# Optimization experiments

Measured on AMD Instinct MI355X. Metric: run time of the kernel, lower is better.

Reference implementation:

```python
import jax, jax.numpy as jnp
from jax import lax
import numpy as np

B, T, D, H, C = 64, 256, 1024, 1024, 27


def _lstm_layer(x, Wih, Whh, bih, bhh):
    """Batch-first LSTM layer matching torch.nn.LSTM gate math.
    x: (N, S, Din) -> returns hs: (N, S, H). Gate order: i, f, g, o."""
    N = x.shape[0]
    Hh = Whh.shape[1]
    # precompute input contribution for all steps: (N, S, 4H)
    xg = jnp.einsum('nsd,gd->nsg', x, Wih) + bih + bhh

    def step(carry, xg_t):
        h, c = carry
        g = xg_t + h @ Whh.T  # (N, 4H)
        i, f, gg, o = jnp.split(g, 4, axis=-1)
        c = jax.nn.sigmoid(f) * c + jax.nn.sigmoid(i) * jnp.tanh(gg)
        h = jax.nn.sigmoid(o) * jnp.tanh(c)
        return (h, c), h

    h0 = jnp.zeros((N, Hh), x.dtype)
    (_, _), hs = lax.scan(step, (h0, h0), jnp.swapaxes(xg, 0, 1))  # scan over S
    return jnp.swapaxes(hs, 0, 1)  # (N, S, H)


def setup_inputs() -> dict:
    key = jax.random.key(0)
    ks = jax.random.split(key, 13)
    s = 1.0 / np.sqrt(H)
    u = lambda k, shape: jax.random.uniform(k, shape, jnp.float32, -s, s)
    return {
        'x': jax.random.normal(ks[0], (B, T, D), jnp.float32),
        'Wih0': u(ks[1], (4 * H, D)), 'Whh0': u(ks[2], (4 * H, H)),
        'bih0': u(ks[3], (4 * H,)), 'bhh0': u(ks[4], (4 * H,)),
        'Wih1': u(ks[5], (4 * H, H)), 'Whh1': u(ks[6], (4 * H, H)),
        'bih1': u(ks[7], (4 * H,)), 'bhh1': u(ks[8], (4 * H,)),
        'W1': u(ks[9], (H // 2, H)), 'b1': u(ks[10], (H // 2,)),
        'W2': u(ks[11], (C, H // 2)), 'b2': u(ks[12], (C,)),
    }


def reference(x, Wih0, Whh0, bih0, bhh0, Wih1, Whh1, bih1, bhh1, W1, b1, W2, b2):
    # Original module permutes (B,T,D) -> (T,B,D) but the LSTM is batch_first,
    # so it treats T as batch and recurs over the original batch axis B.
    xp = jnp.transpose(x, (1, 0, 2))           # (T, B, D): batch=T, seq=B
    h1 = _lstm_layer(xp, Wih0, Whh0, bih0, bhh0)  # (T, B, H)
    h2 = _lstm_layer(h1, Wih1, Whh1, bih1, bhh1)  # (T, B, H)
    out = h2[-1]                                # (B, H): last 'batch' row
    fc = jax.nn.relu(out @ W1.T + b1)
    return fc @ W2.T + b2                       # (B, C)
```

## Files before the change

kernel.cpp:

```cpp
#include <hip/hip_runtime.h>
#include <math.h>


#define NBLK 256
#define TPB  512
#define HDIM 1024
#define SEQ  64
#define GUARD (1L << 20)
#define POISON 0xAAAAAAAAu
#define ENCOFF 0x55555555u

#define WS_H1 0
#define WS_H2 (SEQ * HDIM)
#define WS_FCB (2 * SEQ * HDIM)

#define FMA4(A, W, Hv)                                                         \
  (A).x = fmaf((W).x, (Hv).x, (A).x);                                          \
  (A).y = fmaf((W).y, (Hv).y, (A).y);                                          \
  (A).z = fmaf((W).z, (Hv).z, (A).z);                                          \
  (A).w = fmaf((W).w, (Hv).w, (A).w)

#define PIN4(V)                                                                \
  asm volatile("" : "+v"((V).x), "+v"((V).y), "+v"((V).z), "+v"((V).w))

__device__ __forceinline__ float sigmoidf_(float v) {
  return 1.0f / (1.0f + expf(-v));
}
__device__ __forceinline__ float hsum4(float4 a) {
  return (a.x + a.y) + (a.z + a.w);
}
__device__ __forceinline__ float wave_sum(float v) {
#pragma unroll
  for (int m = 32; m >= 1; m >>= 1) v += __shfl_xor(v, m, 64);
  return v;
}

__device__ __forceinline__ void st_u32(unsigned* p, unsigned v) {
  __hip_atomic_store(p, v, __ATOMIC_RELAXED, __HIP_MEMORY_SCOPE_AGENT);
}
__device__ __forceinline__ unsigned enc(float v) {
  return __float_as_uint(v) + ENCOFF;
}
__device__ __forceinline__ float dec(unsigned u) {
  return __uint_as_float(u - ENCOFF);
}
__device__ __forceinline__ float2 poll2(const unsigned* p) {
  const unsigned long long* pp = (const unsigned long long*)p;
  unsigned lo, hi;
  long g = 0;
  for (;;) {
    unsigned long long u =
        __hip_atomic_load(pp, __ATOMIC_RELAXED, __HIP_MEMORY_SCOPE_AGENT);
    lo = (unsigned)u;
    hi = (unsigned)(u >> 32);
    if ((lo != POISON) & (hi != POISON)) break;
    __builtin_amdgcn_s_sleep(1);
    if (++g > GUARD) break;
  }
  asm volatile("" ::: "memory");
  return make_float2(dec(lo), dec(hi));
}

__global__ void __launch_bounds__(TPB)
__attribute__((amdgpu_waves_per_eu(1, 2)))
lstm_persist(
    const float* __restrict__ x,
    const float* __restrict__ Wih0, const float* __restrict__ Whh0,
    const float* __restrict__ bih0, const float* __restrict__ bhh0,
    const float* __restrict__ Wih1, const float* __restrict__ Whh1,
    const float* __restrict__ bih1, const float* __restrict__ bhh1,
    const float* __restrict__ W1, const float* __restrict__ b1,
    const float* __restrict__ W2, const float* __restrict__ b2,
    float* __restrict__ out, unsigned* ws) {
  __shared__ float sA[2][HDIM];
  __shared__ float sB[2][HDIM];
  __shared__ float sX[2][HDIM];

  unsigned* h1dat = ws + WS_H1;
  unsigned* h2dat = ws + WS_H2;
  unsigned* fcb = ws + WS_FCB;

  const int tid = threadIdx.x;
  const int b = blockIdx.x;
  const int lane = tid & 63;
  const int q = tid >> 6;
  const int L = q >> 2;
  const int elem = (b << 2) + (q & 3);

  const float* Wih = L ? Wih1 : Wih0;
  const float* Whh = L ? Whh1 : Whh0;
  const float* bi = L ? bih1 : bih0;
  const float* bh = L ? bhh1 : bhh0;

  float4 wi[4][4], wr[4][4];
  float bias[4];
#pragma unroll
  for (int g = 0; g < 4; ++g) {
    const int row = (g << 10) + elem;
    bias[g] = bi[row] + bh[row];
    const float4* pi = (const float4*)(Wih + (size_t)row * HDIM);
    const float4* pr = (const float4*)(Whh + (size_t)row * HDIM);
#pragma unroll
    for (int k = 0; k < 4; ++k) {
      wi[g][k] = pi[(k << 6) + lane];
      wr[g][k] = pr[(k << 6) + lane];
    }
  }
#pragma unroll
  for (int g = 0; g < 4; ++g) {
#pragma unroll
    for (int k = 0; k < 4; ++k) {
      PIN4(wi[g][k]);
      PIN4(wr[g][k]);
    }
    asm volatile("" : "+v"(bias[g]));
  }

  float cell = 0.0f;

  for (int p = 0; p <= SEQ; ++p) {
    const int pb = p & 1;
    float2 xv = make_float2(0, 0);
    if (p < SEQ)
      xv = ((const float2*)x)[(size_t)(p * 256 + 255) * 512 + tid];
    float2 vb = make_float2(0, 0);
    if (p >= 2) vb = poll2(h2dat + (size_t)(p - 2) * HDIM + (tid << 1));
    float2 va = make_float2(0, 0);
    if (p >= 1) va = poll2(h1dat + (size_t)(p - 1) * HDIM + (tid << 1));

    ((float2*)sA[pb])[tid] = va;
    ((float2*)sB[pb])[tid] = vb;
    ((float2*)sX[pb])[tid] = xv;
    __syncthreads();

    const float4* A4 = (const float4*)sA[pb];
    const float4* B4 = (const float4*)sB[pb];
    const float4* X4 = (const float4*)sX[pb];

    if (L == 0) {
      if (p < SEQ) {
        float4 acc[4];
#pragma unroll
        for (int g = 0; g < 4; ++g) acc[g] = make_float4(0, 0, 0, 0);
#pragma unroll
        for (int k = 0; k < 4; ++k) {
          float4 xf = X4[(k << 6) + lane];
          float4 hf = A4[(k << 6) + lane];
#pragma unroll
          for (int g = 0; g < 4; ++g) {
            FMA4(acc[g], wi[g][k], xf);
            FMA4(acc[g], wr[g][k], hf);
          }
        }
        float gi = wave_sum(hsum4(acc[0])) + bias[0];
        float gf = wave_sum(hsum4(acc[1])) + bias[1];
        float gg = wave_sum(hsum4(acc[2])) + bias[2];
        float go = wave_sum(hsum4(acc[3])) + bias[3];
        cell = sigmoidf_(gf) * cell + sigmoidf_(gi) * tanhf(gg);
        float hv = sigmoidf_(go) * tanhf(cell);
        if (lane == 0) st_u32(h1dat + (size_t)p * HDIM + elem, enc(hv));
      }
    } else {
      if (p >= 1) {
        float4 acc[4];
#pragma unroll
        for (int g = 0; g < 4; ++g) acc[g] = make_float4(0, 0, 0, 0);
#pragma unroll
        for (int k = 0; k < 4; ++k) {
          float4 iv = A4[(k << 6) + lane];
          float4 hf = B4[(k << 6) + lane];
#pragma unroll
          for (int g = 0; g < 4; ++g) {
            FMA4(acc[g], wi[g][k], iv);
            FMA4(acc[g], wr[g][k], hf);
          }
        }
        float gi = wave_sum(hsum4(acc[0])) + bias[0];
        float gf = wave_sum(hsum4(acc[1])) + bias[1];
        float gg = wave_sum(hsum4(acc[2])) + bias[2];
        float go = wave_sum(hsum4(acc[3])) + bias[3];
        cell = sigmoidf_(gf) * cell + sigmoidf_(gi) * tanhf(gg);
        float hv = sigmoidf_(go) * tanhf(cell);
        if (lane == 0) st_u32(h2dat + (size_t)(p - 1) * HDIM + elem, enc(hv));
      }
    }
  }

  __syncthreads();
  {
    const int s = b >> 2, ch = b & 3;
    float2 v = poll2(h2dat + (size_t)s * HDIM + (tid << 1));
    ((float2*)sA[0])[tid] = v;
    __syncthreads();
    const float4* A4 = (const float4*)sA[0];
    for (int t = 0; t < 16; ++t) {
      const int j = (ch << 7) + (q << 4) + t;
      const float4* w4 = (const float4*)(W1 + (size_t)j * HDIM);
      float4 acc = make_float4(0, 0, 0, 0);
#pragma unroll
      for (int k = 0; k < 4; ++k) {
        float4 wv = w4[(k << 6) + lane];
        float4 hv = A4[(k << 6) + lane];
        FMA4(acc, wv, hv);
      }
      float v2 = wave_sum(hsum4(acc));
      if (lane == 0)
        st_u32(fcb + (size_t)s * 512 + j, enc(fmaxf(v2 + b1[j], 0.0f)));
    }
  }

  if (b < 64) {
    if (tid < 256) {
      float2 v = poll2(fcb + (size_t)b * 512 + (tid << 1));
      ((float2*)sB[0])[tid] = v;
    }
    __syncthreads();
    const float4* B4v = (const float4*)sB[0];
    for (int c = q; c < 27; c += 8) {
      const float4* w4 = (const float4*)(W2 + (size_t)c * 512);
      float4 acc = make_float4(0, 0, 0, 0);
#pragma unroll
      for (int k = 0; k < 2; ++k) {
        float4 wv = w4[(k << 6) + lane];
        float4 hv = B4v[(k << 6) + lane];
        FMA4(acc, wv, hv);
      }
      float v = wave_sum(hsum4(acc));
      if (lane == 0) out[b * 27 + c] = v + b2[c];
    }
  }
}

extern "C" void kernel_launch(void* const* d_in, const int* in_sizes, int n_in,
                              void* d_out, int out_size, void* d_ws,
                              size_t ws_size, hipStream_t stream) {
  (void)in_sizes; (void)n_in; (void)out_size; (void)ws_size;
  const float* x    = (const float*)d_in[0];
  const float* Wih0 = (const float*)d_in[1];
  const float* Whh0 = (const float*)d_in[2];
  const float* bih0 = (const float*)d_in[3];
  const float* bhh0 = (const float*)d_in[4];
  const float* Wih1 = (const float*)d_in[5];
  const float* Whh1 = (const float*)d_in[6];
  const float* bih1 = (const float*)d_in[7];
  const float* bhh1 = (const float*)d_in[8];
  const float* W1   = (const float*)d_in[9];
  const float* b1   = (const float*)d_in[10];
  const float* W2   = (const float*)d_in[11];
  const float* b2   = (const float*)d_in[12];
  float* out = (float*)d_out;
  unsigned* ws = (unsigned*)d_ws;

  hipLaunchKernelGGL(lstm_persist, dim3(NBLK), dim3(TPB), 0, stream, x, Wih0,
                     Whh0, bih0, bhh0, Wih1, Whh1, bih1, bhh1, W1, b1, W2, b2,
                     out, ws);
}
```

Before: 441.8 us.

## Precompute layer-0 input gates upfront and split layer-1 matvec across two waves

Layer-0 input projections for all 64 steps are computed once per block before the recurrence and kept in shared memory, which takes the x·Wih0 work off the serial critical path. Layer-1 rows are now split over two waves per element (K halves), with partial sums combined through shared memory, using 768 threads per block. Each layer-1 wave carries half the weights and FMAs per step, but every step now needs an extra __syncthreads, and the prologue adds up-front work.

```diff
diff --git a/kernel.cpp b/kernel.cpp
--- a/kernel.cpp
+++ b/kernel.cpp
@@ -3,7 +3,7 @@
 
 
 #define NBLK 256
-#define TPB  512
+#define TPB  768
 #define HDIM 1024
 #define SEQ  64
 #define GUARD (1L << 20)
@@ -15,10 +15,12 @@
 #define WS_FCB (2 * SEQ * HDIM)
 
 #define FMA4(A, W, Hv)                                                         \
-  (A).x = fmaf((W).x, (Hv).x, (A).x);                                          \
-  (A).y = fmaf((W).y, (Hv).y, (A).y);                                          \
-  (A).z = fmaf((W).z, (Hv).z, (A).z);                                          \
-  (A).w = fmaf((W).w, (Hv).w, (A).w)
+  do {                                                                         \
+    (A).x = fmaf((W).x, (Hv).x, (A).x);                                        \
+    (A).y = fmaf((W).y, (Hv).y, (A).y);                                        \
+    (A).z = fmaf((W).z, (Hv).z, (A).z);                                        \
+    (A).w = fmaf((W).w, (Hv).w, (A).w);                                        \
+  } while (0)
 
 #define PIN4(V)                                                                \
   asm volatile("" : "+v"((V).x), "+v"((V).y), "+v"((V).z), "+v"((V).w))
@@ -60,9 +62,26 @@
   asm volatile("" ::: "memory");
   return make_float2(dec(lo), dec(hi));
 }
+__device__ __forceinline__ float4 poll4(const unsigned* p) {
+  const unsigned long long* pp = (const unsigned long long*)p;
+  unsigned long long u0, u1;
+  long g = 0;
+  for (;;) {
+    u0 = __hip_atomic_load(pp, __ATOMIC_RELAXED, __HIP_MEMORY_SCOPE_AGENT);
+    u1 = __hip_atomic_load(pp + 1, __ATOMIC_RELAXED, __HIP_MEMORY_SCOPE_AGENT);
+    if (((unsigned)u0 != POISON) & ((unsigned)(u0 >> 32) != POISON) &
+        ((unsigned)u1 != POISON) & ((unsigned)(u1 >> 32) != POISON))
+      break;
+    __builtin_amdgcn_s_sleep(1);
+    if (++g > GUARD) break;
+  }
+  asm volatile("" ::: "memory");
+  return make_float4(dec((unsigned)u0), dec((unsigned)(u0 >> 32)),
+                     dec((unsigned)u1), dec((unsigned)(u1 >> 32)));
+}
 
 __global__ void __launch_bounds__(TPB)
-__attribute__((amdgpu_waves_per_eu(1, 2)))
+__attribute__((amdgpu_waves_per_eu(1, 3)))
 lstm_persist(
     const float* __restrict__ x,
     const float* __restrict__ Wih0, const float* __restrict__ Whh0,
@@ -74,7 +93,8 @@
     float* __restrict__ out, unsigned* ws) {
   __shared__ float sA[2][HDIM];
   __shared__ float sB[2][HDIM];
-  __shared__ float sX[2][HDIM];
+  __shared__ float xg[16][SEQ];
+  __shared__ float sP[4][4];
 
   unsigned* h1dat = ws + WS_H1;
   unsigned* h2dat = ws + WS_H2;
@@ -84,119 +104,152 @@
   const int b = blockIdx.x;
   const int lane = tid & 63;
   const int q = tid >> 6;
-  const int L = q >> 2;
-  const int elem = (b << 2) + (q & 3);
-
-  const float* Wih = L ? Wih1 : Wih0;
-  const float* Whh = L ? Whh1 : Whh0;
-  const float* bi = L ? bih1 : bih0;
-  const float* bh = L ? bhh1 : bhh0;
-
-  float4 wi[4][4], wr[4][4];
-  float bias[4];
+  const int L = (q >= 4);
+  const int idx = q - 4;
+  const int e = (L == 0) ? q : (idx >> 1);
+  const int kh = idx & 1;
+  const int elem = (b << 2) + e;
+
+  float4 wgt[4][4];
+  float bias1[4] = {0.f, 0.f, 0.f, 0.f};
+  if (L == 0) {
+#pragma unroll
+    for (int g = 0; g < 4; ++g) {
+      const int row = (g << 10) + elem;
+      const float4* pr = (const float4*)(Whh0 + (size_t)row * HDIM);
+#pragma unroll
+      for (int k = 0; k < 4; ++k) wgt[g][k] = pr[(k << 6) + lane];
+    }
+  } else {
+#pragma unroll
+    for (int g = 0; g < 4; ++g) {
+      const int row = (g << 10) + elem;
+      bias1[g] = bih1[row] + bhh1[row];
+      const float4* pi = (const float4*)(Wih1 + (size_t)row * HDIM);
+      const float4* pr = (const float4*)(Whh1 + (size_t)row * HDIM);
+#pragma unroll
+      for (int k = 0; k < 2; ++k) {
+        const int c = (kh << 1) + k;
+        wgt[g][k] = pi[(c << 6) + lane];
+        wgt[g][k + 2] = pr[(c << 6) + lane];
+      }
+    }
+  }
 #pragma unroll
   for (int g = 0; g < 4; ++g) {
-    const int row = (g << 10) + elem;
-    bias[g] = bi[row] + bh[row];
-    const float4* pi = (const float4*)(Wih + (size_t)row * HDIM);
-    const float4* pr = (const float4*)(Whh + (size_t)row * HDIM);
-#pragma unroll
-    for (int k = 0; k < 4; ++k) {
-      wi[g][k] = pi[(k << 6) + lane];
-      wr[g][k] = pr[(k << 6) + lane];
-    }
-  }
-#pragma unroll
-  for (int g = 0; g < 4; ++g) {
-#pragma unroll
-    for (int k = 0; k < 4; ++k) {
-      PIN4(wi[g][k]);
-      PIN4(wr[g][k]);
-    }
-    asm volatile("" : "+v"(bias[g]));
-  }
+#pragma unroll
+    for (int k = 0; k < 4; ++k) PIN4(wgt[g][k]);
+    asm volatile("" : "+v"(bias1[g]));
+  }
+
+  for (int r = q; r < 16; r += 12) {
+    const int g = r >> 2, ee = r & 3;
+    const int grow = (g << 10) + (b << 2) + ee;
+    const float4* wrow = (const float4*)(Wih0 + (size_t)grow * HDIM);
+    const float4* xrow =
+        (const float4*)(x + (size_t)(lane * 256 + 255) * HDIM);
+    float4 acc = make_float4(0.f, 0.f, 0.f, 0.f);
+#pragma unroll 4
+    for (int kk = 0; kk < 256; ++kk) {
+      float4 wv = wrow[kk];
+      float4 xv = xrow[kk];
+      FMA4(acc, wv, xv);
+    }
+    xg[r][lane] = hsum4(acc) + bih0[grow] + bhh0[grow];
+  }
+  __syncthreads();
 
   float cell = 0.0f;
 
   for (int p = 0; p <= SEQ; ++p) {
     const int pb = p & 1;
-    float2 xv = make_float2(0, 0);
-    if (p < SEQ)
-      xv = ((const float2*)x)[(size_t)(p * 256 + 255) * 512 + tid];
-    float2 vb = make_float2(0, 0);
-    if (p >= 2) vb = poll2(h2dat + (size_t)(p - 2) * HDIM + (tid << 1));
-    float2 va = make_float2(0, 0);
-    if (p >= 1) va = poll2(h1dat + (size_t)(p - 1) * HDIM + (tid << 1));
-
-    ((float2*)sA[pb])[tid] = va;
-    ((float2*)sB[pb])[tid] = vb;
-    ((float2*)sX[pb])[tid] = xv;
+    if (tid < 512) {
+      float2 va = make_float2(0.f, 0.f);
+      if (p >= 1) va = poll2(h1dat + (size_t)(p - 1) * HDIM + (tid << 1));
+      ((float2*)sA[pb])[tid] = va;
+    } else {
+      const int t = tid - 512;
+      float4 vb = make_float4(0.f, 0.f, 0.f, 0.f);
+      if (p >= 2) vb = poll4(h2dat + (size_t)(p - 2) * HDIM + (t << 2));
+      ((float4*)sB[pb])[t] = vb;
+    }
     __syncthreads();
 
     const float4* A4 = (const float4*)sA[pb];
     const float4* B4 = (const float4*)sB[pb];
-    const float4* X4 = (const float4*)sX[pb];
+    float part[4] = {0.f, 0.f, 0.f, 0.f};
 
     if (L == 0) {
       if (p < SEQ) {
         float4 acc[4];
 #pragma unroll
-        for (int g = 0; g < 4; ++g) acc[g] = make_float4(0, 0, 0, 0);
+        for (int g = 0; g < 4; ++g) acc[g] = make_float4(0.f, 0.f, 0.f, 0.f);
 #pragma unroll
         for (int k = 0; k < 4; ++k) {
-          float4 xf = X4[(k << 6) + lane];
           float4 hf = A4[(k << 6) + lane];
 #pragma unroll
           for (int g = 0; g < 4; ++g) {
-            FMA4(acc[g], wi[g][k], xf);
-            FMA4(acc[g], wr[g][k], hf);
+            FMA4(acc[g], wgt[g][k], hf);
           }
         }
-        float gi = wave_sum(hsum4(acc[0])) + bias[0];
-        float gf = wave_sum(hsum4(acc[1])) + bias[1];
-        float gg = wave_sum(hsum4(acc[2])) + bias[2];
-        float go = wave_sum(hsum4(acc[3])) + bias[3];
+        float gi = wave_sum(hsum4(acc[0])) + xg[(0 << 2) + e][p];
+        float gf = wave_sum(hsum4(acc[1])) + xg[(1 << 2) + e][p];
+        float gg = wave_sum(hsum4(acc[2])) + xg[(2 << 2) + e][p];
+        float go = wave_sum(hsum4(acc[3])) + xg[(3 << 2) + e][p];
         cell = sigmoidf_(gf) * cell + sigmoidf_(gi) * tanhf(gg);
         float hv = sigmoidf_(go) * tanhf(cell);
         if (lane == 0) st_u32(h1dat + (size_t)p * HDIM + elem, enc(hv));
       }
-    } else {
-      if (p >= 1) {
-        float4 acc[4];
-#pragma unroll
-        for (int g = 0; g < 4; ++g) acc[g] = make_float4(0, 0, 0, 0);
-#pragma unroll
-        for (int k = 0; k < 4; ++k) {
-          float4 iv = A4[(k << 6) + lane];
-          float4 hf = B4[(k << 6) + lane];
-#pragma unroll
-          for (int g = 0; g < 4; ++g) {
-            FMA4(acc[g], wi[g][k], iv);
-            FMA4(acc[g], wr[g][k], hf);
-          }
+    } else if (p >= 1) {
+      float4 acc[4];
+#pragma unroll
+      for (int g = 0; g < 4; ++g) acc[g] = make_float4(0.f, 0.f, 0.f, 0.f);
+#pragma unroll
+      for (int k = 0; k < 2; ++k) {
+        const int c = (kh << 1) + k;
+        float4 iv = A4[(c << 6) + lane];
+        float4 hf = B4[(c << 6) + lane];
+#pragma unroll
+        for (int g = 0; g < 4; ++g) {
+          FMA4(acc[g], wgt[g][k], iv);
+          FMA4(acc[g], wgt[g][k + 2], hf);
         }
-        float gi = wave_sum(hsum4(acc[0])) + bias[0];
-        float gf = wave_sum(hsum4(acc[1])) + bias[1];
-        float gg = wave_sum(hsum4(acc[2])) + bias[2];
-        float go = wave_sum(hsum4(acc[3])) + bias[3];
-        cell = sigmoidf_(gf) * cell + sigmoidf_(gi) * tanhf(gg);
-        float hv = sigmoidf_(go) * tanhf(cell);
-        if (lane == 0) st_u32(h2dat + (size_t)(p - 1) * HDIM + elem, enc(hv));
-      }
+      }
+#pragma unroll
+      for (int g = 0; g < 4; ++g) part[g] = wave_sum(hsum4(acc[g]));
+      if (kh == 1 && lane == 0) {
+        sP[e][0] = part[0];
+        sP[e][1] = part[1];
+        sP[e][2] = part[2];
+        sP[e][3] = part[3];
+      }
+    }
+    __syncthreads();
+
+    if (L == 1 && kh == 0 && p >= 1) {
+      float gi = part[0] + sP[e][0] + bias1[0];
+      float gf = part[1] + sP[e][1] + bias1[1];
+      float gg = part[2] + sP[e][2] + bias1[2];
+      float go = part[3] + sP[e][3] + bias1[3];
+      cell = sigmoidf_(gf) * cell + sigmoidf_(gi) * tanhf(gg);
+      float hv = sigmoidf_(go) * tanhf(cell);
+      if (lane == 0) st_u32(h2dat + (size_t)(p - 1) * HDIM + elem, enc(hv));
     }
   }
 
   __syncthreads();
   {
     const int s = b >> 2, ch = b & 3;
-    float2 v = poll2(h2dat + (size_t)s * HDIM + (tid << 1));
-    ((float2*)sA[0])[tid] = v;
+    if (tid < 512) {
+      float2 v = poll2(h2dat + (size_t)s * HDIM + (tid << 1));
+      ((float2*)sA[0])[tid] = v;
+    }
     __syncthreads();
     const float4* A4 = (const float4*)sA[0];
-    for (int t = 0; t < 16; ++t) {
-      const int j = (ch << 7) + (q << 4) + t;
+    for (int j0 = q; j0 < 128; j0 += 12) {
+      const int j = (ch << 7) + j0;
       const float4* w4 = (const float4*)(W1 + (size_t)j * HDIM);
-      float4 acc = make_float4(0, 0, 0, 0);
+      float4 acc = make_float4(0.f, 0.f, 0.f, 0.f);
 #pragma unroll
       for (int k = 0; k < 4; ++k) {
         float4 wv = w4[(k << 6) + lane];
@@ -216,9 +269,9 @@
     }
     __syncthreads();
     const float4* B4v = (const float4*)sB[0];
-    for (int c = q; c < 27; c += 8) {
+    for (int c = q; c < 27; c += 12) {
       const float4* w4 = (const float4*)(W2 + (size_t)c * 512);
-      float4 acc = make_float4(0, 0, 0, 0);
+      float4 acc = make_float4(0.f, 0.f, 0.f, 0.f);
 #pragma unroll
       for (int k = 0; k < 2; ++k) {
         float4 wv = w4[(k << 6) + lane];
```

Result: slower. 648.8 us (+46.8%).
